# Kernel tuning notes

Hardware: AMD Instinct MI355X
Metric: run time of the kernel (lower is better)

Reference implementation:

```python
import jax, jax.numpy as jnp
import numpy as np

B, C, H, W = 64, 2048, 14, 14
D, S, ITERS, EPS, HID = 256, 8, 3, 1e-8, 512


def build_pos(h, w, d):
    gy, gx = np.meshgrid(np.arange(h), np.arange(w), indexing='ij')
    q = d // 4
    omega = 1.0 / (10000.0 ** (np.arange(q) / q))
    ey = gy.reshape(-1, 1) * omega
    ex = gx.reshape(-1, 1) * omega
    pe = np.concatenate([np.sin(ey), np.cos(ey), np.sin(ex), np.cos(ex)], axis=1)
    return jnp.asarray(pe[None], jnp.float32)  # (1, h*w, d)


def layernorm(x, g, b, eps=1e-5):
    m = x.mean(-1, keepdims=True)
    v = ((x - m) ** 2).mean(-1, keepdims=True)
    return (x - m) * jax.lax.rsqrt(v + eps) * g + b


def setup_inputs() -> dict:
    key = jax.random.key(0)
    ks = jax.random.split(key, 16)
    w = lambda k, shp, s=0.02: jax.random.normal(k, shp, jnp.float32) * s
    inp = {
        'x': jax.random.normal(ks[0], (B, C, H, W), jnp.float32),
        'slot_noise': jax.random.normal(ks[1], (B, S, D), jnp.float32),
        'conv_w': w(ks[2], (C, D)), 'conv_b': jnp.zeros((D,), jnp.float32),
        'pos': build_pos(H, W, D),
        'slots_mu': jax.random.normal(ks[3], (1, 1, D), jnp.float32),
        'slots_logsigma': -jnp.ones((1, 1, D), jnp.float32),
        'qw': w(ks[4], (D, D)), 'qb': jnp.zeros((D,), jnp.float32),
        'kw': w(ks[5], (D, D)), 'kb': jnp.zeros((D,), jnp.float32),
        'vw': w(ks[6], (D, D)), 'vb': jnp.zeros((D,), jnp.float32),
        'gru_wih': w(ks[7], (D, 3 * D)), 'gru_whh': w(ks[8], (D, 3 * D)),
        'gru_bih': jnp.zeros((3 * D,), jnp.float32), 'gru_bhh': jnp.zeros((3 * D,), jnp.float32),
        'w1': w(ks[9], (D, HID)), 'b1': jnp.zeros((HID,), jnp.float32),
        'w2': w(ks[10], (HID, D)), 'b2': jnp.zeros((D,), jnp.float32),
        'ln_in_g': jnp.ones((D,), jnp.float32), 'ln_in_b': jnp.zeros((D,), jnp.float32),
        'ln_s_g': jnp.ones((D,), jnp.float32), 'ln_s_b': jnp.zeros((D,), jnp.float32),
        'ln_ff_g': jnp.ones((D,), jnp.float32), 'ln_ff_b': jnp.zeros((D,), jnp.float32),
    }
    return inp


def reference(x, slot_noise, conv_w, conv_b, pos, slots_mu, slots_logsigma,
              qw, qb, kw, kb, vw, vb, gru_wih, gru_whh, gru_bih, gru_bhh,
              w1, b1, w2, b2, ln_in_g, ln_in_b, ln_s_g, ln_s_b, ln_ff_g, ln_ff_b):
    b, c, h, w_ = x.shape
    d = qw.shape[0]
    scale = d ** (-0.5)
    # (B,C,H,W) -> (B,N,C) -> project -> add pos
    xt = x.transpose(0, 2, 3, 1).reshape(b, h * w_, c)
    xt = xt @ conv_w + conv_b + pos
    # slot init
    slots = slots_mu + jnp.exp(slots_logsigma) * slot_noise  # (B,S,D)
    inp = layernorm(xt, ln_in_g, ln_in_b)
    k = inp @ kw + kb
    v = inp @ vw + vb
    attn = None
    for _ in range(ITERS):
        slots_prev = slots
        s = layernorm(slots, ln_s_g, ln_s_b)
        q = s @ qw + qb
        dots = jnp.einsum('bid,bjd->bij', q, k) * scale  # (B,S,N)
        attn = jax.nn.softmax(dots, axis=1) + EPS  # softmax over slots
        attn = attn / attn.sum(-1, keepdims=True)  # renormalize over keys
        updates = jnp.einsum('bjd,bij->bid', v, attn)  # (B,S,D)
        # GRUCell (torch semantics)
        gi = updates @ gru_wih + gru_bih
        gh = slots_prev @ gru_whh + gru_bhh
        ir, iz, inn = jnp.split(gi, 3, axis=-1)
        hr, hz, hn = jnp.split(gh, 3, axis=-1)
        r = jax.nn.sigmoid(ir + hr)
        z = jax.nn.sigmoid(iz + hz)
        nn_ = jnp.tanh(inn + r * hn)
        slots = (1.0 - z) * nn_ + z * slots_prev
        ff = layernorm(slots, ln_ff_g, ln_ff_b)
        slots = slots + (jax.nn.relu(ff @ w1 + b1)) @ w2 + b2
    attn_map = attn.reshape(b, S, h, w_)
    return slots, attn_map
```

## Files before the change

### kernel.cpp

```cpp
#include <hip/hip_runtime.h>
#include <stdint.h>

#define HWN 196
#define CIN 2048
#define DD  256
#define BB  64
#define NSLOT 8
#define KVPAD 224
#define MTOT 12544
#define BKP 128

typedef __attribute__((ext_vector_type(8))) short short8;
typedef __attribute__((ext_vector_type(4))) float f32x4;
typedef __attribute__((ext_vector_type(4))) unsigned short us4;

__device__ __forceinline__ ushort f2bf(float f){ union{float f;uint32_t u;}v;v.f=f;uint32_t u=v.u;return (ushort)((u+0x7FFFu+((u>>16)&1u))>>16);}
__device__ __forceinline__ float bf2f(ushort h){ union{uint32_t u;float f;}v;v.u=((uint32_t)h)<<16;return v.f;}
__device__ __forceinline__ float sigm(float x){ return 1.f/(1.f+expf(-x)); }

__device__ __forceinline__ short8 ldsY(const ushort* buf, int LD, int kt, int lane){
    int row = lane & 15;
    int ch = kt*4 + (lane>>4);
    return *(const short8*)&buf[row*LD + ((ch ^ (row&7))<<3)];
}
__device__ __forceinline__ short8 gX(const ushort* base, int K, int nrow, int kt, int lane){
    return *(const short8*)&base[(size_t)nrow*K + kt*32 + (lane>>4)*8];
}

struct TD { const float* s; ushort* d; int R, C, t0; };
struct TD8 { TD a[8]; };

__global__ __launch_bounds__(256) void k_prep(TD8 td){
    __shared__ float tile[32][33];
    int bt = blockIdx.x;
    int mi = 0;
    #pragma unroll
    for (int i = 1; i < 8; ++i) if (bt >= td.a[i].t0) mi = i;
    TD d = td.a[mi];
    int lt = bt - d.t0;
    int tilesx = (d.C + 31) >> 5;
    int cb = (lt % tilesx) * 32, rb = (lt / tilesx) * 32;
    int tx = threadIdx.x & 31, ty = threadIdx.x >> 5;
    for (int i = ty; i < 32; i += 8) {
        int r = rb + i, c = cb + tx;
        tile[i][tx] = (r < d.R && c < d.C) ? d.s[(size_t)r * d.C + c] : 0.f;
    }
    __syncthreads();
    for (int i = ty; i < 32; i += 8) {
        int c = cb + i, r = rb + tx;
        if (c < d.C && r < d.R) d.d[(size_t)c * d.R + r] = f2bf(tile[tx][i]);
    }
}

__global__ __launch_bounds__(512) void k_proj(const float* __restrict__ x,
        const ushort* __restrict__ cwT, float* __restrict__ Cpart,
        int SK, int ksteps){
    __shared__ ushort As[2][64*BKP];
    const int t = threadIdx.x, lane = t & 63, wv = t >> 6;
    const int tile = blockIdx.x / SK, kq = blockIdx.x % SK;
    const int bm = tile * 64;
    const int kbase = kq * (ksteps * BKP);

    const int am = t & 63, kg = t >> 6;
    const int mg = bm + am;
    const int ab = mg / HWN, ap = mg % HWN;
    const float* aptr = x + (size_t)ab*(CIN*HWN) + ap + (size_t)kbase*HWN;

    f32x4 acc[4][2] = {};
    float areg[16];

    #pragma unroll
    for (int j = 0; j < 16; ++j) areg[j] = aptr[(size_t)(kg*16+j)*HWN];
    {
        short8 av0, av1;
        #pragma unroll
        for (int j = 0; j < 8; ++j){ av0[j] = (short)f2bf(areg[j]); av1[j] = (short)f2bf(areg[8+j]); }
        int ch0 = kg*2;
        *(short8*)&As[0][am*BKP + ((ch0^(am&7))<<3)] = av0;
        *(short8*)&As[0][am*BKP + (((ch0+1)^(am&7))<<3)] = av1;
    }
    __syncthreads();
    int cur = 0;
    for (int kt = 0; kt < ksteps; ++kt){
        if (kt < ksteps-1){
            #pragma unroll
            for (int j = 0; j < 16; ++j)
                areg[j] = aptr[(size_t)((kt+1)*BKP + kg*16+j)*HWN];
        }
        short8 bfr[4][2];
        #pragma unroll
        for (int kk = 0; kk < 4; ++kk)
            #pragma unroll
            for (int ni = 0; ni < 2; ++ni){
                int n = wv*32 + ni*16 + (lane&15);
                bfr[kk][ni] = *(const short8*)&cwT[(size_t)n*CIN + kbase + kt*BKP + kk*32 + (lane>>4)*8];
            }
        #pragma unroll
        for (int kk = 0; kk < 4; ++kk){
            short8 afr[4];
            #pragma unroll
            for (int mi = 0; mi < 4; ++mi){
                int row = mi*16 + (lane&15);
                int ch = kk*4 + (lane>>4);
                afr[mi] = *(const short8*)&As[cur][row*BKP + ((ch^(row&7))<<3)];
            }
            #pragma unroll
            for (int mi = 0; mi < 4; ++mi)
                #pragma unroll
                for (int ni = 0; ni < 2; ++ni)
                    acc[mi][ni] = __builtin_amdgcn_mfma_f32_16x16x32_bf16(afr[mi], bfr[kk][ni], acc[mi][ni], 0,0,0);
        }
        if (kt < ksteps-1){
            short8 av0, av1;
            #pragma unroll
            for (int j = 0; j < 8; ++j){ av0[j] = (short)f2bf(areg[j]); av1[j] = (short)f2bf(areg[8+j]); }
            int ch0 = kg*2;
            *(short8*)&As[cur^1][am*BKP + ((ch0^(am&7))<<3)] = av0;
            *(short8*)&As[cur^1][am*BKP + (((ch0+1)^(am&7))<<3)] = av1;
        }
        __syncthreads();
        cur ^= 1;
    }
    float* outp = Cpart + (size_t)kq*MTOT*DD;
    #pragma unroll
    for (int mi = 0; mi < 4; ++mi){
        #pragma unroll
        for (int ni = 0; ni < 2; ++ni){
            int n = wv*32 + ni*16 + (lane&15);
            #pragma unroll
            for (int r = 0; r < 4; ++r){
                int m = bm + mi*16 + (lane>>4)*4 + r;
                outp[(size_t)m*DD + n] = acc[mi][ni][r];
            }
        }
    }
}

__global__ __launch_bounds__(512) void k_red(const float* __restrict__ Cpart, int SK,
        const float* __restrict__ cb, const float* __restrict__ pos,
        const float* __restrict__ lng, const float* __restrict__ lnb,
        const ushort* __restrict__ kwT, const ushort* __restrict__ vwT,
        const float* __restrict__ kb, const float* __restrict__ vb,
        ushort* __restrict__ kbf, ushort* __restrict__ vT){
    __shared__ ushort As[32*256];
    const int t = threadIdx.x, lane = t & 63, wv = t >> 6;
    const int b = blockIdx.x / 7, pblk = blockIdx.x % 7;
    {
        int row = t >> 4, seg = t & 15;
        int pin = pblk*32 + row;
        int grow = b*HWN + pin;
        if (grow > MTOT-1) grow = MTOT-1;
        int p = pin < HWN ? pin : HWN-1;
        const float* pp = pos + (size_t)p*DD + seg*16;
        float f[16];
        #pragma unroll
        for (int q = 0; q < 4; ++q){
            f32x4 pv = *(const f32x4*)&pp[q*4];
            f32x4 cv = *(const f32x4*)&cb[seg*16 + q*4];
            #pragma unroll
            for (int r2 = 0; r2 < 4; ++r2) f[q*4+r2] = pv[r2] + cv[r2];
        }
        for (int sk = 0; sk < SK; ++sk){
            const float* cp = Cpart + (size_t)sk*MTOT*DD + (size_t)grow*DD + seg*16;
            #pragma unroll
            for (int q = 0; q < 4; ++q){
                f32x4 a = *(const f32x4*)&cp[q*4];
                #pragma unroll
                for (int r2 = 0; r2 < 4; ++r2) f[q*4+r2] += a[r2];
            }
        }
        float s = 0.f, sq = 0.f;
        #pragma unroll
        for (int j = 0; j < 16; ++j){ s += f[j]; sq += f[j]*f[j]; }
        #pragma unroll
        for (int m = 8; m >= 1; m >>= 1){ s += __shfl_xor(s, m, 64); sq += __shfl_xor(sq, m, 64); }
        float mean = s * (1.f/256.f);
        float rs = rsqrtf(sq*(1.f/256.f) - mean*mean + 1e-5f);
        int d0 = seg*16;
        short8 o0, o1;
        #pragma unroll
        for (int j = 0; j < 8; ++j){
            o0[j] = (short)f2bf((f[j]   - mean)*rs*lng[d0+j]   + lnb[d0+j]);
            o1[j] = (short)f2bf((f[8+j] - mean)*rs*lng[d0+8+j] + lnb[d0+8+j]);
        }
        int ch0 = seg*2;
        *(short8*)&As[row*256 + ((ch0^(row&7))<<3)] = o0;
        *(short8*)&As[row*256 + (((ch0+1)^(row&7))<<3)] = o1;
    }
    __syncthreads();
    f32x4 acck[2][2] = {}, accv[2][2] = {};
    const int n0 = wv*32;
    #pragma unroll
    for (int kt = 0; kt < 8; ++kt){
        short8 afr[2];
        #pragma unroll
        for (int mi = 0; mi < 2; ++mi){
            int row = mi*16 + (lane&15);
            int ch = kt*4 + (lane>>4);
            afr[mi] = *(const short8*)&As[row*256 + ((ch^(row&7))<<3)];
        }
        #pragma unroll
        for (int ni = 0; ni < 2; ++ni){
            int n = n0 + ni*16 + (lane&15);
            int koff = kt*32 + (lane>>4)*8;
            short8 bk = *(const short8*)&kwT[(size_t)n*DD + koff];
            short8 bv = *(const short8*)&vwT[(size_t)n*DD + koff];
            #pragma unroll
            for (int mi = 0; mi < 2; ++mi){
                acck[mi][ni] = __builtin_amdgcn_mfma_f32_16x16x32_bf16(afr[mi], bk, acck[mi][ni],0,0,0);
                accv[mi][ni] = __builtin_amdgcn_mfma_f32_16x16x32_bf16(afr[mi], bv, accv[mi][ni],0,0,0);
            }
        }
    }
    #pragma unroll
    for (int mi = 0; mi < 2; ++mi){
        #pragma unroll
        for (int ni = 0; ni < 2; ++ni){
            int n = n0 + ni*16 + (lane&15);
            float kbn = kb[n], vbn = vb[n];
            int pl0 = pblk*32 + mi*16 + (lane>>4)*4;
            us4 pk;
            #pragma unroll
            for (int r = 0; r < 4; ++r){
                kbf[((size_t)b*KVPAD + pl0 + r)*DD + n] = f2bf(acck[mi][ni][r] + kbn);
                pk[r] = f2bf(accv[mi][ni][r] + vbn);
            }
            *(us4*)&vT[((size_t)b*DD + n)*KVPAD + pl0] = pk;
        }
    }
}

__global__ __launch_bounds__(512) void k_init(const float* __restrict__ noise,
        const float* __restrict__ mu, const float* __restrict__ lsig,
        const ushort* __restrict__ qwT, const float* __restrict__ qb,
        const float* __restrict__ gs, const float* __restrict__ bs,
        float* __restrict__ slots, ushort* __restrict__ qbuf){
    __shared__ float Sld[16*256];
    __shared__ ushort Ysn[16*256];
    __shared__ float part[8][16][2];
    __shared__ float stats[16][2];
    const int t = threadIdx.x, lane = t & 63, w = t >> 6;
    const int bb = blockIdx.x, rbase = bb*16;
    {
        int row = t>>5, ch = t&31; int d = ch*8;
        f32x4 n0 = *(const f32x4*)&noise[(size_t)(rbase+row)*DD + d];
        f32x4 n1 = *(const f32x4*)&noise[(size_t)(rbase+row)*DD + d + 4];
        f32x4 m0 = *(const f32x4*)&mu[d];
        f32x4 m1 = *(const f32x4*)&mu[d+4];
        f32x4 l0 = *(const f32x4*)&lsig[d];
        f32x4 l1 = *(const f32x4*)&lsig[d+4];
        f32x4 s0, s1;
        #pragma unroll
        for (int j = 0; j < 4; ++j){
            s0[j] = m0[j] + expf(l0[j])*n0[j];
            s1[j] = m1[j] + expf(l1[j])*n1[j];
        }
        *(f32x4*)&slots[(size_t)(rbase+row)*DD + d] = s0;
        *(f32x4*)&slots[(size_t)(rbase+row)*DD + d + 4] = s1;
        *(f32x4*)&Sld[row*256 + d] = s0;
        *(f32x4*)&Sld[row*256 + d + 4] = s1;
    }
    __syncthreads();
    f32x4 sv[2];
    #pragma unroll
    for (int sub = 0; sub < 2; ++sub){
        int d0 = w*32 + sub*16 + (lane>>4)*4;
        sv[sub] = *(const f32x4*)&Sld[(lane&15)*256 + d0];
    }
    {
        float lsum = 0.f, lsq = 0.f;
        #pragma unroll
        for (int sub = 0; sub < 2; ++sub)
            #pragma unroll
            for (int r = 0; r < 4; ++r){ float v = sv[sub][r]; lsum += v; lsq += v*v; }
        lsum += __shfl_xor(lsum, 16, 64); lsum += __shfl_xor(lsum, 32, 64);
        lsq  += __shfl_xor(lsq, 16, 64);  lsq  += __shfl_xor(lsq, 32, 64);
        if (lane < 16){ part[w][lane][0] = lsum; part[w][lane][1] = lsq; }
    }
    __syncthreads();
    if (t < 16){
        float a = 0.f, c = 0.f;
        #pragma unroll
        for (int i = 0; i < 8; ++i){ a += part[i][t][0]; c += part[i][t][1]; }
        float mean = a*(1.f/256.f);
        stats[t][0] = mean;
        stats[t][1] = rsqrtf(c*(1.f/256.f) - mean*mean + 1e-5f);
    }
    __syncthreads();
    {
        int slot = lane&15;
        float mean = stats[slot][0], rs = stats[slot][1];
        #pragma unroll
        for (int sub = 0; sub < 2; ++sub){
            int d0 = w*32 + sub*16 + (lane>>4)*4;
            f32x4 g4 = *(const f32x4*)&gs[d0];
            f32x4 b4 = *(const f32x4*)&bs[d0];
            us4 o;
            #pragma unroll
            for (int r = 0; r < 4; ++r) o[r] = f2bf((sv[sub][r]-mean)*rs*g4[r] + b4[r]);
            int ch = d0>>3;
            *(us4*)&Ysn[slot*256 + ((ch^(slot&7))<<3) + (d0&7)] = o;
        }
    }
    __syncthreads();
    f32x4 qa[2] = {};
    #pragma unroll
    for (int kt = 0; kt < 8; ++kt){
        short8 ysn = ldsY(Ysn, 256, kt, lane);
        #pragma unroll
        for (int sub = 0; sub < 2; ++sub){
            int nrow = w*32 + sub*16 + (lane&15);
            short8 xx = gX(qwT, 256, nrow, kt, lane);
            qa[sub] = __builtin_amdgcn_mfma_f32_16x16x32_bf16(xx, ysn, qa[sub], 0,0,0);
        }
    }
    #pragma unroll
    for (int sub = 0; sub < 2; ++sub){
        int qd0 = w*32 + sub*16 + (lane>>4)*4;
        f32x4 qb4 = *(const f32x4*)&qb[qd0];
        us4 o;
        #pragma unroll
        for (int r = 0; r < 4; ++r) o[r] = f2bf((qa[sub][r]+qb4[r])*0.0625f);
        *(us4*)&qbuf[(size_t)(rbase+(lane&15))*DD + qd0] = o;
    }
}

__device__ __forceinline__ float sm_ep(f32x4 acc, int f, int lane, ushort* Xat, int srow){
    int k0 = f*16 + (lane>>4)*4;
    us4 o;
    float ps = 0.f;
    #pragma unroll
    for (int r = 0; r < 4; ++r){
        float v = acc[r];
        float mx = v;
        mx = fmaxf(mx, __shfl_xor(mx, 1, 64));
        mx = fmaxf(mx, __shfl_xor(mx, 2, 64));
        mx = fmaxf(mx, __shfl_xor(mx, 4, 64));
        float e = expf(v - mx);
        float se = e;
        se += __shfl_xor(se, 1, 64);
        se += __shfl_xor(se, 2, 64);
        se += __shfl_xor(se, 4, 64);
        float val = e/se + 1e-8f;
        if (k0 + r >= HWN) val = 0.f;
        ps += val;
        o[r] = f2bf(val);
    }
    int ch = k0 >> 3;
    *(us4*)&Xat[srow*256 + ((ch^(srow&7))<<3) + (k0&7)] = o;
    return ps;
}

__global__ __launch_bounds__(1024, 4) void k_slot(
        const ushort* __restrict__ qbuf, const ushort* __restrict__ kbf,
        const ushort* __restrict__ vT, float* __restrict__ slots,
        ushort* __restrict__ qout,
        const ushort* __restrict__ wihT, const ushort* __restrict__ whhT,
        const float* __restrict__ bih, const float* __restrict__ bhh,
        const ushort* __restrict__ w1T, const float* __restrict__ b1,
        const ushort* __restrict__ w2T, const float* __restrict__ b2,
        const float* __restrict__ gff, const float* __restrict__ bff,
        const float* __restrict__ gs, const float* __restrict__ bs,
        const ushort* __restrict__ qwT, const float* __restrict__ qb,
        float* __restrict__ out_slots, float* __restrict__ out_attn,
        int final_){
    __shared__ ushort Yq[16*256];
    __shared__ ushort Xat[16*256];
    __shared__ ushort Yupd[16*256];
    __shared__ ushort Yslb[16*256];
    __shared__ ushort Ysn[16*256];
    __shared__ ushort Yh[16*512];
    __shared__ float wpart[16][16];
    __shared__ float invk[16];
    __shared__ float part[16][16][2];
    __shared__ float stats[16][2];
    const int t = threadIdx.x, lane = t & 63, w = t >> 6;
    const int b = blockIdx.x;
    const int rbase = b * NSLOT;
    const int srow = lane & 15;
    const int srd = (srow < NSLOT) ? srow : 0;

    if (t < 256){
        int row = t>>5, ch = t&31;
        short8 v = *(const short8*)&qbuf[(size_t)(rbase+row)*DD + ch*8];
        *(short8*)&Yq[row*256 + ((ch^(row&7))<<3)] = v;
        f32x4 s0 = *(const f32x4*)&slots[(size_t)(rbase+row)*DD + ch*8];
        f32x4 s1 = *(const f32x4*)&slots[(size_t)(rbase+row)*DD + ch*8 + 4];
        short8 sv;
        #pragma unroll
        for (int j = 0; j < 4; ++j){ sv[j] = (short)f2bf(s0[j]); sv[4+j] = (short)f2bf(s1[j]); }
        *(short8*)&Yslb[row*256 + ((ch^(row&7))<<3)] = sv;
    } else if (t < 512){
        int i = t - 256;
        int row = (i>>5) + 8, ch = i&31;
        short8 z;
        #pragma unroll
        for (int j = 0; j < 8; ++j) z[j] = 0;
        *(short8*)&Yq[row*256 + ((ch^(row&7))<<3)] = z;
        *(short8*)&Yupd[row*256 + ((ch^(row&7))<<3)] = z;
        *(short8*)&Yslb[row*256 + ((ch^(row&7))<<3)] = z;
    }
    __syncthreads();
    if (w < 14){
        short8 yf[8];
        #pragma unroll
        for (int kt = 0; kt < 8; ++kt) yf[kt] = ldsY(Yq, 256, kt, lane);
        const ushort* kb_ = kbf + (size_t)b*KVPAD*DD;
        const int r0 = w*16 + (lane&15);
        short8 xa[2];
        xa[0] = gX(kb_, 256, r0, 0, lane);
        f32x4 accA = {};
        #pragma unroll
        for (int kt = 0; kt < 8; ++kt){
            int cu = kt & 1, nx = cu ^ 1;
            if (kt < 7) xa[nx] = gX(kb_, 256, r0, kt+1, lane);
            accA = __builtin_amdgcn_mfma_f32_16x16x32_bf16(xa[cu], yf[kt], accA, 0,0,0);
        }
        float ps = sm_ep(accA, w, lane, Xat, srow);
        ps += __shfl_xor(ps, 16, 64);
        ps += __shfl_xor(ps, 32, 64);
        if (lane < 16) wpart[w][lane] = ps;
    } else {
        if (lane < 16) wpart[w][lane] = 0.f;
    }
    __syncthreads();
    if (t < 16){
        float s = 0.f;
        #pragma unroll
        for (int i = 0; i < 16; ++i) s += wpart[i][t];
        invk[t] = 1.f/s;
    }
    f32x4 pv;
    {
        short8 xat[7];
        #pragma unroll
        for (int kt = 0; kt < 7; ++kt) xat[kt] = ldsY(Xat, 256, kt, lane);
        const ushort* vb_ = vT + (size_t)b*DD*KVPAD;
        const int d0r = w*16 + (lane&15);
        short8 ya[2];
        ya[0] = gX(vb_, KVPAD, d0r, 0, lane);
        f32x4 aA = {};
        #pragma unroll
        for (int kt = 0; kt < 7; ++kt){
            int cu = kt & 1, nx = cu ^ 1;
            if (kt < 6) ya[nx] = gX(vb_, KVPAD, d0r, kt+1, lane);
            aA = __builtin_amdgcn_mfma_f32_16x16x32_bf16(xat[kt], ya[cu], aA, 0,0,0);
        }
        pv = aA;
    }
    __syncthreads();
    {
        f32x4 iv = *(const f32x4*)&invk[(lane>>4)*4];
        int d0 = w*16;
        #pragma unroll
        for (int r = 0; r < 4; ++r){
            int s2 = (lane>>4)*4 + r;
            if (s2 < NSLOT){
                int d = d0 + (lane&15);
                int ch = d >> 3;
                Yupd[s2*256 + ((ch^(s2&7))<<3) + (d&7)] = f2bf(pv[r]*iv[r]);
            }
        }
    }
    if (final_){
        for (int idx = t; idx < NSLOT*HWN; idx += 1024){
            int slot = idx/HWN, key = idx - slot*HWN;
            int ch = key >> 3;
            out_attn[(size_t)b*NSLOT*HWN + idx] =
                bf2f(Xat[slot*256 + ((ch^(slot&7))<<3) + (key&7)]) * invk[slot];
        }
    }
    __syncthreads();
    f32x4 gi[3] = {}, gh[3] = {};
    {
        int nrw[3];
        #pragma unroll
        for (int g = 0; g < 3; ++g) nrw[g] = g*256 + w*16 + (lane&15);
        short8 xw[2][6];
        #pragma unroll
        for (int g = 0; g < 3; ++g){
            xw[0][g]   = gX(wihT, 256, nrw[g], 0, lane);
            xw[0][3+g] = gX(whhT, 256, nrw[g], 0, lane);
        }
        #pragma unroll
        for (int kt = 0; kt < 8; ++kt){
            int cu = kt & 1, nx = cu ^ 1;
            if (kt < 7){
                #pragma unroll
                for (int g = 0; g < 3; ++g){
                    xw[nx][g]   = gX(wihT, 256, nrw[g], kt+1, lane);
                    xw[nx][3+g] = gX(whhT, 256, nrw[g], kt+1, lane);
                }
            }
            short8 yu = ldsY(Yupd, 256, kt, lane);
            short8 ys = ldsY(Yslb, 256, kt, lane);
            #pragma unroll
            for (int g = 0; g < 3; ++g){
                gi[g] = __builtin_amdgcn_mfma_f32_16x16x32_bf16(xw[cu][g],   yu, gi[g], 0,0,0);
                gh[g] = __builtin_amdgcn_mfma_f32_16x16x32_bf16(xw[cu][3+g], ys, gh[g], 0,0,0);
            }
        }
    }
    f32x4 snew;
    {
        int d0 = w*16 + (lane>>4)*4;
        f32x4 sp  = *(const f32x4*)&slots[(size_t)(rbase + srd)*DD + d0];
        f32x4 bir = *(const f32x4*)&bih[d0];
        f32x4 biz = *(const f32x4*)&bih[256 + d0];
        f32x4 bin = *(const f32x4*)&bih[512 + d0];
        f32x4 bhr = *(const f32x4*)&bhh[d0];
        f32x4 bhz = *(const f32x4*)&bhh[256 + d0];
        f32x4 bhn = *(const f32x4*)&bhh[512 + d0];
        #pragma unroll
        for (int r = 0; r < 4; ++r){
            float ir = gi[0][r] + bir[r];
            float iz = gi[1][r] + biz[r];
            float in_ = gi[2][r] + bin[r];
            float hr = gh[0][r] + bhr[r];
            float hz = gh[1][r] + bhz[r];
            float hn = gh[2][r] + bhn[r];
            float rr = sigm(ir + hr);
            float zz = sigm(iz + hz);
            float nn = tanhf(in_ + rr*hn);
            snew[r] = (1.f - zz)*nn + zz*sp[r];
        }
    }
    {
        float lsum = 0.f, lsq = 0.f;
        #pragma unroll
        for (int r = 0; r < 4; ++r){ float v = snew[r]; lsum += v; lsq += v*v; }
        lsum += __shfl_xor(lsum, 16, 64); lsum += __shfl_xor(lsum, 32, 64);
        lsq  += __shfl_xor(lsq, 16, 64);  lsq  += __shfl_xor(lsq, 32, 64);
        if (lane < 16){ part[w][lane][0] = lsum; part[w][lane][1] = lsq; }
    }
    __syncthreads();
    if (t < 16){
        float a = 0.f, c = 0.f;
        #pragma unroll
        for (int i = 0; i < 16; ++i){ a += part[i][t][0]; c += part[i][t][1]; }
        float mean = a*(1.f/256.f);
        stats[t][0] = mean;
        stats[t][1] = rsqrtf(c*(1.f/256.f) - mean*mean + 1e-5f);
    }
    __syncthreads();
    {
        float mean = stats[srow][0], rs = stats[srow][1];
        int d0 = w*16 + (lane>>4)*4;
        f32x4 g4 = *(const f32x4*)&gff[d0];
        f32x4 b4 = *(const f32x4*)&bff[d0];
        us4 o;
        #pragma unroll
        for (int r = 0; r < 4; ++r) o[r] = f2bf((snew[r]-mean)*rs*g4[r] + b4[r]);
        int ch = d0 >> 3;
        *(us4*)&Ysn[srow*256 + ((ch^(srow&7))<<3) + (d0&7)] = o;
    }
    __syncthreads();
    {
        int nr1[2];
        #pragma unroll
        for (int s2 = 0; s2 < 2; ++s2) nr1[s2] = w*32 + s2*16 + (lane&15);
        short8 xw1[2][2];
        #pragma unroll
        for (int s2 = 0; s2 < 2; ++s2) xw1[0][s2] = gX(w1T, 256, nr1[s2], 0, lane);
        f32x4 hh[2] = {};
        #pragma unroll
        for (int kt = 0; kt < 8; ++kt){
            int cu = kt & 1, nx = cu ^ 1;
            if (kt < 7){
                #pragma unroll
                for (int s2 = 0; s2 < 2; ++s2) xw1[nx][s2] = gX(w1T, 256, nr1[s2], kt+1, lane);
            }
            short8 ysn = ldsY(Ysn, 256, kt, lane);
            #pragma unroll
            for (int s2 = 0; s2 < 2; ++s2)
                hh[s2] = __builtin_amdgcn_mfma_f32_16x16x32_bf16(xw1[cu][s2], ysn, hh[s2], 0,0,0);
        }
        #pragma unroll
        for (int s2 = 0; s2 < 2; ++s2){
            int n0 = w*32 + s2*16 + (lane>>4)*4;
            f32x4 b14 = *(const f32x4*)&b1[n0];
            us4 o;
            #pragma unroll
            for (int r = 0; r < 4; ++r) o[r] = f2bf(fmaxf(hh[s2][r] + b14[r], 0.f));
            int ch = n0 >> 3;
            *(us4*)&Yh[srow*512 + ((ch^(srow&7))<<3) + (n0&7)] = o;
        }
    }
    __syncthreads();
    f32x4 ns;
    {
        int nr2 = w*16 + (lane&15);
        short8 xw2[2];
        xw2[0] = gX(w2T, 512, nr2, 0, lane);
        f32x4 o2 = {};
        #pragma unroll
        for (int kt = 0; kt < 16; ++kt){
            int cu = kt & 1, nx = cu ^ 1;
            if (kt < 15) xw2[nx] = gX(w2T, 512, nr2, kt+1, lane);
            short8 yh = ldsY(Yh, 512, kt, lane);
            o2 = __builtin_amdgcn_mfma_f32_16x16x32_bf16(xw2[cu], yh, o2, 0,0,0);
        }
        float* dst = final_ ? out_slots : slots;
        int d0 = w*16 + (lane>>4)*4;
        f32x4 b24 = *(const f32x4*)&b2[d0];
        #pragma unroll
        for (int r = 0; r < 4; ++r) ns[r] = o2[r] + b24[r] + snew[r];
        if (srow < NSLOT)
            *(f32x4*)&dst[(size_t)(rbase + srow)*DD + d0] = ns;
    }
    if (final_) return;
    {
        float lsum = 0.f, lsq = 0.f;
        #pragma unroll
        for (int r = 0; r < 4; ++r){ float v = ns[r]; lsum += v; lsq += v*v; }
        lsum += __shfl_xor(lsum, 16, 64); lsum += __shfl_xor(lsum, 32, 64);
        lsq  += __shfl_xor(lsq, 16, 64);  lsq  += __shfl_xor(lsq, 32, 64);
        if (lane < 16){ part[w][lane][0] = lsum; part[w][lane][1] = lsq; }
    }
    __syncthreads();
    if (t < 16){
        float a = 0.f, c = 0.f;
        #pragma unroll
        for (int i = 0; i < 16; ++i){ a += part[i][t][0]; c += part[i][t][1]; }
        float mean = a*(1.f/256.f);
        stats[t][0] = mean;
        stats[t][1] = rsqrtf(c*(1.f/256.f) - mean*mean + 1e-5f);
    }
    __syncthreads();
    {
        float mean = stats[srow][0], rs = stats[srow][1];
        int d0 = w*16 + (lane>>4)*4;
        f32x4 g4 = *(const f32x4*)&gs[d0];
        f32x4 b4 = *(const f32x4*)&bs[d0];
        us4 o;
        #pragma unroll
        for (int r = 0; r < 4; ++r) o[r] = f2bf((ns[r]-mean)*rs*g4[r] + b4[r]);
        int ch = d0 >> 3;
        *(us4*)&Ysn[srow*256 + ((ch^(srow&7))<<3) + (d0&7)] = o;
    }
    __syncthreads();
    {
        int nrq = w*16 + (lane&15);
        short8 xq[2];
        xq[0] = gX(qwT, 256, nrq, 0, lane);
        f32x4 qa = {};
        #pragma unroll
        for (int kt = 0; kt < 8; ++kt){
            int cu = kt & 1, nx = cu ^ 1;
            if (kt < 7) xq[nx] = gX(qwT, 256, nrq, kt+1, lane);
            short8 ysn = ldsY(Ysn, 256, kt, lane);
            qa = __builtin_amdgcn_mfma_f32_16x16x32_bf16(xq[cu], ysn, qa, 0,0,0);
        }
        int qd0 = w*16 + (lane>>4)*4;
        f32x4 qb4 = *(const f32x4*)&qb[qd0];
        us4 o;
        #pragma unroll
        for (int r = 0; r < 4; ++r) o[r] = f2bf((qa[r]+qb4[r])*0.0625f);
        if (srow < NSLOT)
            *(us4*)&qout[(size_t)(rbase + srow)*DD + qd0] = o;
    }
}

extern "C" void kernel_launch(void* const* d_in, const int* in_sizes, int n_in,
                              void* d_out, int out_size, void* d_ws, size_t ws_size,
                              hipStream_t stream) {
    const float* x      = (const float*)d_in[0];
    const float* noise  = (const float*)d_in[1];
    const float* conv_w = (const float*)d_in[2];
    const float* conv_b = (const float*)d_in[3];
    const float* pos    = (const float*)d_in[4];
    const float* mu     = (const float*)d_in[5];
    const float* logsig = (const float*)d_in[6];
    const float* qw  = (const float*)d_in[7];
    const float* qb  = (const float*)d_in[8];
    const float* kw  = (const float*)d_in[9];
    const float* kb  = (const float*)d_in[10];
    const float* vw  = (const float*)d_in[11];
    const float* vb  = (const float*)d_in[12];
    const float* wih = (const float*)d_in[13];
    const float* whh = (const float*)d_in[14];
    const float* bih = (const float*)d_in[15];
    const float* bhh = (const float*)d_in[16];
    const float* w1  = (const float*)d_in[17];
    const float* b1  = (const float*)d_in[18];
    const float* w2  = (const float*)d_in[19];
    const float* b2  = (const float*)d_in[20];
    const float* g_in = (const float*)d_in[21];
    const float* b_in = (const float*)d_in[22];
    const float* g_s  = (const float*)d_in[23];
    const float* b_s  = (const float*)d_in[24];
    const float* g_ff = (const float*)d_in[25];
    const float* b_ff = (const float*)d_in[26];

    char* w = (char*)d_ws;
    ushort* kbf    = (ushort*)w; w += (size_t)BB*KVPAD*DD*2;
    ushort* vT     = (ushort*)w; w += (size_t)BB*DD*KVPAD*2;
    ushort* cwT    = (ushort*)w; w += (size_t)DD*CIN*2;
    ushort* qwT    = (ushort*)w; w += (size_t)DD*DD*2;
    ushort* kwT    = (ushort*)w; w += (size_t)DD*DD*2;
    ushort* vwT    = (ushort*)w; w += (size_t)DD*DD*2;
    ushort* wihT   = (ushort*)w; w += (size_t)768*DD*2;
    ushort* whhT   = (ushort*)w; w += (size_t)768*DD*2;
    ushort* w1T    = (ushort*)w; w += (size_t)512*DD*2;
    ushort* w2T    = (ushort*)w; w += (size_t)DD*512*2;
    ushort* qbb    = (ushort*)w; w += (size_t)BB*NSLOT*DD*2;
    float*  slotsb = (float*)w;  w += (size_t)BB*NSLOT*DD*4;
    float*  Cpart  = (float*)w;
    size_t fixedBytes = (size_t)(w - (char*)d_ws);
    int SK = (fixedBytes + (size_t)4*MTOT*DD*4 <= ws_size) ? 4 : 2;
    int ksteps = 16 / SK;

    float* out_slots = (float*)d_out;
    float* out_attn  = (float*)d_out + (size_t)BB*NSLOT*DD;

    TD8 td;
    td.a[0] = { conv_w, cwT, 2048, 256,    0 };
    td.a[1] = { qw,     qwT,  256, 256,  512 };
    td.a[2] = { kw,     kwT,  256, 256,  576 };
    td.a[3] = { vw,     vwT,  256, 256,  640 };
    td.a[4] = { wih,    wihT, 256, 768,  704 };
    td.a[5] = { whh,    whhT, 256, 768,  896 };
    td.a[6] = { w1,     w1T,  256, 512, 1088 };
    td.a[7] = { w2,     w2T,  512, 256, 1216 };

    k_prep<<<1344, 256, 0, stream>>>(td);
    k_proj<<<196*SK, 512, 0, stream>>>(x, cwT, Cpart, SK, ksteps);
    k_red<<<448, 512, 0, stream>>>(Cpart, SK, conv_b, pos, g_in, b_in,
                                   kwT, vwT, kb, vb, kbf, vT);
    k_init<<<32, 512, 0, stream>>>(noise, mu, logsig, qwT, qb, g_s, b_s, slotsb, qbb);
    for (int it = 0; it < 3; ++it){
        k_slot<<<BB, 1024, 0, stream>>>(qbb, kbf, vT, slotsb, qbb,
                                        wihT, whhT, bih, bhh, w1T, b1, w2T, b2,
                                        g_ff, b_ff, g_s, b_s, qwT, qb,
                                        out_slots, out_attn, it == 2);
    }
}
```

Before: 243.5 us.

## Replace split-K projection with N-tiled GEMM and merge kv/init kernels

The conv projection GEMM no longer splits K and writes fp32 partials. It tiles over N in two 128-wide halves, runs the full K loop, and writes a bf16 xt with bias and positional encoding already added. The K/V layernorm-projection kernel and the slot-init kernel are merged into one launch. In k_slot, several stats and inverse-sum stages now compute redundantly per thread, which removes __syncthreads, and the occupancy hint is lowered. This cuts partial-sum traffic and a launch, but drops the register double-buffering in k_proj and adds bf16 rounding of xt before the layernorm.

```diff
diff --git a/kernel.cpp b/kernel.cpp
--- a/kernel.cpp
+++ b/kernel.cpp
@@ -8,7 +8,6 @@
 #define NSLOT 8
 #define KVPAD 224
 #define MTOT 12544
-#define BKP 128
 
 typedef __attribute__((ext_vector_type(8))) short short8;
 typedef __attribute__((ext_vector_type(4))) float f32x4;
@@ -52,276 +51,260 @@
     }
 }
 
-__global__ __launch_bounds__(512) void k_proj(const float* __restrict__ x,
-        const ushort* __restrict__ cwT, float* __restrict__ Cpart,
-        int SK, int ksteps){
-    __shared__ ushort As[2][64*BKP];
-    const int t = threadIdx.x, lane = t & 63, wv = t >> 6;
-    const int tile = blockIdx.x / SK, kq = blockIdx.x % SK;
-    const int bm = tile * 64;
-    const int kbase = kq * (ksteps * BKP);
-
-    const int am = t & 63, kg = t >> 6;
+__global__ __launch_bounds__(256) void k_proj(const float* __restrict__ x,
+        const ushort* __restrict__ bT, const float* __restrict__ cb,
+        const float* __restrict__ pos, ushort* __restrict__ xt){
+    __shared__ ushort As[64 * 64];
+    __shared__ ushort Bs[128 * 64];
+    const int t = threadIdx.x;
+    const int lane = t & 63;
+    const int wv = t >> 6;
+    const int wm = wv >> 1, wn = wv & 1;
+    const int bm = blockIdx.x * 64;
+    const int bn = blockIdx.y * 128;
+
+    const int am = t & 63;
     const int mg = bm + am;
     const int ab = mg / HWN, ap = mg % HWN;
-    const float* aptr = x + (size_t)ab*(CIN*HWN) + ap + (size_t)kbase*HWN;
-
-    f32x4 acc[4][2] = {};
-    float areg[16];
-
+    const float* aptr = x + (size_t)ab * (CIN * HWN) + ap;
+    const int achb = t >> 6;
+
+    const int bnl = t >> 1;
+    const int bch0 = (t & 1) * 4;
+    const ushort* bptr = bT + (size_t)(bn + bnl) * CIN;
+
+    f32x4 acc[2][4] = {};
+
+    for (int k0 = 0; k0 < CIN; k0 += 64) {
+        if (k0) __syncthreads();
+        #pragma unroll
+        for (int p = 0; p < 2; ++p) {
+            int ch = achb + 4 * p;
+            short8 av;
+            #pragma unroll
+            for (int j = 0; j < 8; ++j)
+                av[j] = (short)f2bf(aptr[(size_t)(k0 + ch * 8 + j) * HWN]);
+            *(short8*)&As[am * 64 + ((ch ^ (am & 7)) << 3)] = av;
+        }
+        #pragma unroll
+        for (int c = 0; c < 4; ++c) {
+            int ch = bch0 + c;
+            short8 bv = *(const short8*)&bptr[k0 + ch * 8];
+            *(short8*)&Bs[bnl * 64 + ((ch ^ (bnl & 7)) << 3)] = bv;
+        }
+        __syncthreads();
+        #pragma unroll
+        for (int kk = 0; kk < 2; ++kk) {
+            short8 afr[2], bfr[4];
+            #pragma unroll
+            for (int mi = 0; mi < 2; ++mi) {
+                int row = wm * 32 + mi * 16 + (lane & 15);
+                int ch = kk * 4 + (lane >> 4);
+                afr[mi] = *(const short8*)&As[row * 64 + ((ch ^ (row & 7)) << 3)];
+            }
+            #pragma unroll
+            for (int ni = 0; ni < 4; ++ni) {
+                int row = wn * 64 + ni * 16 + (lane & 15);
+                int ch = kk * 4 + (lane >> 4);
+                bfr[ni] = *(const short8*)&Bs[row * 64 + ((ch ^ (row & 7)) << 3)];
+            }
+            #pragma unroll
+            for (int mi = 0; mi < 2; ++mi)
+                #pragma unroll
+                for (int ni = 0; ni < 4; ++ni)
+                    acc[mi][ni] = __builtin_amdgcn_mfma_f32_16x16x32_bf16(
+                        afr[mi], bfr[ni], acc[mi][ni], 0, 0, 0);
+        }
+    }
     #pragma unroll
-    for (int j = 0; j < 16; ++j) areg[j] = aptr[(size_t)(kg*16+j)*HWN];
-    {
-        short8 av0, av1;
-        #pragma unroll
-        for (int j = 0; j < 8; ++j){ av0[j] = (short)f2bf(areg[j]); av1[j] = (short)f2bf(areg[8+j]); }
-        int ch0 = kg*2;
-        *(short8*)&As[0][am*BKP + ((ch0^(am&7))<<3)] = av0;
-        *(short8*)&As[0][am*BKP + (((ch0+1)^(am&7))<<3)] = av1;
-    }
-    __syncthreads();
-    int cur = 0;
-    for (int kt = 0; kt < ksteps; ++kt){
-        if (kt < ksteps-1){
-            #pragma unroll
-            for (int j = 0; j < 16; ++j)
-                areg[j] = aptr[(size_t)((kt+1)*BKP + kg*16+j)*HWN];
-        }
-        short8 bfr[4][2];
-        #pragma unroll
-        for (int kk = 0; kk < 4; ++kk)
-            #pragma unroll
-            for (int ni = 0; ni < 2; ++ni){
-                int n = wv*32 + ni*16 + (lane&15);
-                bfr[kk][ni] = *(const short8*)&cwT[(size_t)n*CIN + kbase + kt*BKP + kk*32 + (lane>>4)*8];
-            }
-        #pragma unroll
-        for (int kk = 0; kk < 4; ++kk){
-            short8 afr[4];
-            #pragma unroll
-            for (int mi = 0; mi < 4; ++mi){
-                int row = mi*16 + (lane&15);
-                int ch = kk*4 + (lane>>4);
-                afr[mi] = *(const short8*)&As[cur][row*BKP + ((ch^(row&7))<<3)];
-            }
-            #pragma unroll
-            for (int mi = 0; mi < 4; ++mi)
-                #pragma unroll
-                for (int ni = 0; ni < 2; ++ni)
-                    acc[mi][ni] = __builtin_amdgcn_mfma_f32_16x16x32_bf16(afr[mi], bfr[kk][ni], acc[mi][ni], 0,0,0);
-        }
-        if (kt < ksteps-1){
-            short8 av0, av1;
-            #pragma unroll
-            for (int j = 0; j < 8; ++j){ av0[j] = (short)f2bf(areg[j]); av1[j] = (short)f2bf(areg[8+j]); }
-            int ch0 = kg*2;
-            *(short8*)&As[cur^1][am*BKP + ((ch0^(am&7))<<3)] = av0;
-            *(short8*)&As[cur^1][am*BKP + (((ch0+1)^(am&7))<<3)] = av1;
-        }
-        __syncthreads();
-        cur ^= 1;
-    }
-    float* outp = Cpart + (size_t)kq*MTOT*DD;
-    #pragma unroll
-    for (int mi = 0; mi < 4; ++mi){
-        #pragma unroll
-        for (int ni = 0; ni < 2; ++ni){
-            int n = wv*32 + ni*16 + (lane&15);
-            #pragma unroll
-            for (int r = 0; r < 4; ++r){
-                int m = bm + mi*16 + (lane>>4)*4 + r;
-                outp[(size_t)m*DD + n] = acc[mi][ni][r];
+    for (int mi = 0; mi < 2; ++mi) {
+        #pragma unroll
+        for (int ni = 0; ni < 4; ++ni) {
+            int n = bn + wn * 64 + ni * 16 + (lane & 15);
+            float cbn = cb[n];
+            #pragma unroll
+            for (int r = 0; r < 4; ++r) {
+                int row = wm * 32 + mi * 16 + (lane >> 4) * 4 + r;
+                int m = bm + row;
+                int p = m % HWN;
+                xt[(size_t)m * DD + n] = f2bf(acc[mi][ni][r] + cbn + pos[(size_t)p * DD + n]);
             }
         }
     }
 }
 
-__global__ __launch_bounds__(512) void k_red(const float* __restrict__ Cpart, int SK,
-        const float* __restrict__ cb, const float* __restrict__ pos,
-        const float* __restrict__ lng, const float* __restrict__ lnb,
+__global__ __launch_bounds__(512) void k_kvinit(const ushort* __restrict__ xt,
         const ushort* __restrict__ kwT, const ushort* __restrict__ vwT,
         const float* __restrict__ kb, const float* __restrict__ vb,
-        ushort* __restrict__ kbf, ushort* __restrict__ vT){
-    __shared__ ushort As[32*256];
-    const int t = threadIdx.x, lane = t & 63, wv = t >> 6;
-    const int b = blockIdx.x / 7, pblk = blockIdx.x % 7;
-    {
-        int row = t >> 4, seg = t & 15;
-        int pin = pblk*32 + row;
-        int grow = b*HWN + pin;
-        if (grow > MTOT-1) grow = MTOT-1;
-        int p = pin < HWN ? pin : HWN-1;
-        const float* pp = pos + (size_t)p*DD + seg*16;
-        float f[16];
-        #pragma unroll
-        for (int q = 0; q < 4; ++q){
-            f32x4 pv = *(const f32x4*)&pp[q*4];
-            f32x4 cv = *(const f32x4*)&cb[seg*16 + q*4];
-            #pragma unroll
-            for (int r2 = 0; r2 < 4; ++r2) f[q*4+r2] = pv[r2] + cv[r2];
-        }
-        for (int sk = 0; sk < SK; ++sk){
-            const float* cp = Cpart + (size_t)sk*MTOT*DD + (size_t)grow*DD + seg*16;
-            #pragma unroll
-            for (int q = 0; q < 4; ++q){
-                f32x4 a = *(const f32x4*)&cp[q*4];
-                #pragma unroll
-                for (int r2 = 0; r2 < 4; ++r2) f[q*4+r2] += a[r2];
-            }
-        }
-        float s = 0.f, sq = 0.f;
-        #pragma unroll
-        for (int j = 0; j < 16; ++j){ s += f[j]; sq += f[j]*f[j]; }
-        #pragma unroll
-        for (int m = 8; m >= 1; m >>= 1){ s += __shfl_xor(s, m, 64); sq += __shfl_xor(sq, m, 64); }
-        float mean = s * (1.f/256.f);
-        float rs = rsqrtf(sq*(1.f/256.f) - mean*mean + 1e-5f);
-        int d0 = seg*16;
-        short8 o0, o1;
-        #pragma unroll
-        for (int j = 0; j < 8; ++j){
-            o0[j] = (short)f2bf((f[j]   - mean)*rs*lng[d0+j]   + lnb[d0+j]);
-            o1[j] = (short)f2bf((f[8+j] - mean)*rs*lng[d0+8+j] + lnb[d0+8+j]);
-        }
-        int ch0 = seg*2;
-        *(short8*)&As[row*256 + ((ch0^(row&7))<<3)] = o0;
-        *(short8*)&As[row*256 + (((ch0+1)^(row&7))<<3)] = o1;
-    }
-    __syncthreads();
-    f32x4 acck[2][2] = {}, accv[2][2] = {};
-    const int n0 = wv*32;
-    #pragma unroll
-    for (int kt = 0; kt < 8; ++kt){
-        short8 afr[2];
-        #pragma unroll
-        for (int mi = 0; mi < 2; ++mi){
-            int row = mi*16 + (lane&15);
-            int ch = kt*4 + (lane>>4);
-            afr[mi] = *(const short8*)&As[row*256 + ((ch^(row&7))<<3)];
-        }
-        #pragma unroll
-        for (int ni = 0; ni < 2; ++ni){
-            int n = n0 + ni*16 + (lane&15);
-            int koff = kt*32 + (lane>>4)*8;
-            short8 bk = *(const short8*)&kwT[(size_t)n*DD + koff];
-            short8 bv = *(const short8*)&vwT[(size_t)n*DD + koff];
-            #pragma unroll
-            for (int mi = 0; mi < 2; ++mi){
-                acck[mi][ni] = __builtin_amdgcn_mfma_f32_16x16x32_bf16(afr[mi], bk, acck[mi][ni],0,0,0);
-                accv[mi][ni] = __builtin_amdgcn_mfma_f32_16x16x32_bf16(afr[mi], bv, accv[mi][ni],0,0,0);
-            }
-        }
-    }
-    #pragma unroll
-    for (int mi = 0; mi < 2; ++mi){
-        #pragma unroll
-        for (int ni = 0; ni < 2; ++ni){
-            int n = n0 + ni*16 + (lane&15);
-            float kbn = kb[n], vbn = vb[n];
-            int pl0 = pblk*32 + mi*16 + (lane>>4)*4;
-            us4 pk;
-            #pragma unroll
-            for (int r = 0; r < 4; ++r){
-                kbf[((size_t)b*KVPAD + pl0 + r)*DD + n] = f2bf(acck[mi][ni][r] + kbn);
-                pk[r] = f2bf(accv[mi][ni][r] + vbn);
-            }
-            *(us4*)&vT[((size_t)b*DD + n)*KVPAD + pl0] = pk;
-        }
-    }
-}
-
-__global__ __launch_bounds__(512) void k_init(const float* __restrict__ noise,
-        const float* __restrict__ mu, const float* __restrict__ lsig,
+        const float* __restrict__ lng, const float* __restrict__ lnb,
+        ushort* __restrict__ kbf, ushort* __restrict__ vT,
+        const float* __restrict__ noise, const float* __restrict__ mu,
+        const float* __restrict__ lsig,
         const ushort* __restrict__ qwT, const float* __restrict__ qb,
         const float* __restrict__ gs, const float* __restrict__ bs,
         float* __restrict__ slots, ushort* __restrict__ qbuf){
+    __shared__ ushort As[32*256];
     __shared__ float Sld[16*256];
-    __shared__ ushort Ysn[16*256];
     __shared__ float part[8][16][2];
     __shared__ float stats[16][2];
-    const int t = threadIdx.x, lane = t & 63, w = t >> 6;
-    const int bb = blockIdx.x, rbase = bb*16;
-    {
-        int row = t>>5, ch = t&31; int d = ch*8;
-        f32x4 n0 = *(const f32x4*)&noise[(size_t)(rbase+row)*DD + d];
-        f32x4 n1 = *(const f32x4*)&noise[(size_t)(rbase+row)*DD + d + 4];
-        f32x4 m0 = *(const f32x4*)&mu[d];
-        f32x4 m1 = *(const f32x4*)&mu[d+4];
-        f32x4 l0 = *(const f32x4*)&lsig[d];
-        f32x4 l1 = *(const f32x4*)&lsig[d+4];
-        f32x4 s0, s1;
-        #pragma unroll
-        for (int j = 0; j < 4; ++j){
-            s0[j] = m0[j] + expf(l0[j])*n0[j];
-            s1[j] = m1[j] + expf(l1[j])*n1[j];
-        }
-        *(f32x4*)&slots[(size_t)(rbase+row)*DD + d] = s0;
-        *(f32x4*)&slots[(size_t)(rbase+row)*DD + d + 4] = s1;
-        *(f32x4*)&Sld[row*256 + d] = s0;
-        *(f32x4*)&Sld[row*256 + d + 4] = s1;
-    }
-    __syncthreads();
-    f32x4 sv[2];
-    #pragma unroll
-    for (int sub = 0; sub < 2; ++sub){
-        int d0 = w*32 + sub*16 + (lane>>4)*4;
-        sv[sub] = *(const f32x4*)&Sld[(lane&15)*256 + d0];
-    }
-    {
-        float lsum = 0.f, lsq = 0.f;
-        #pragma unroll
-        for (int sub = 0; sub < 2; ++sub)
-            #pragma unroll
-            for (int r = 0; r < 4; ++r){ float v = sv[sub][r]; lsum += v; lsq += v*v; }
-        lsum += __shfl_xor(lsum, 16, 64); lsum += __shfl_xor(lsum, 32, 64);
-        lsq  += __shfl_xor(lsq, 16, 64);  lsq  += __shfl_xor(lsq, 32, 64);
-        if (lane < 16){ part[w][lane][0] = lsum; part[w][lane][1] = lsq; }
-    }
-    __syncthreads();
-    if (t < 16){
-        float a = 0.f, c = 0.f;
-        #pragma unroll
-        for (int i = 0; i < 8; ++i){ a += part[i][t][0]; c += part[i][t][1]; }
-        float mean = a*(1.f/256.f);
-        stats[t][0] = mean;
-        stats[t][1] = rsqrtf(c*(1.f/256.f) - mean*mean + 1e-5f);
-    }
-    __syncthreads();
-    {
-        int slot = lane&15;
-        float mean = stats[slot][0], rs = stats[slot][1];
+    const int t = threadIdx.x, lane = t & 63, wv = t >> 6;
+    if (blockIdx.x < 448){
+        const int b = blockIdx.x / 7, pblk = blockIdx.x % 7;
+        {
+            int row = t >> 4, seg = t & 15;
+            int grow = b*HWN + pblk*32 + row;
+            if (grow > MTOT-1) grow = MTOT-1;
+            const ushort* src = &xt[(size_t)grow*DD + seg*16];
+            short8 v0 = *(const short8*)&src[0];
+            short8 v1 = *(const short8*)&src[8];
+            float f[16];
+            #pragma unroll
+            for (int j = 0; j < 8; ++j){ f[j] = bf2f((ushort)v0[j]); f[8+j] = bf2f((ushort)v1[j]); }
+            float s = 0.f, sq = 0.f;
+            #pragma unroll
+            for (int j = 0; j < 16; ++j){ s += f[j]; sq += f[j]*f[j]; }
+            #pragma unroll
+            for (int m = 8; m >= 1; m >>= 1){ s += __shfl_xor(s, m, 64); sq += __shfl_xor(sq, m, 64); }
+            float mean = s * (1.f/256.f);
+            float rs = rsqrtf(sq*(1.f/256.f) - mean*mean + 1e-5f);
+            int d0 = seg*16;
+            short8 o0, o1;
+            #pragma unroll
+            for (int j = 0; j < 8; ++j){
+                o0[j] = (short)f2bf((f[j]   - mean)*rs*lng[d0+j]   + lnb[d0+j]);
+                o1[j] = (short)f2bf((f[8+j] - mean)*rs*lng[d0+8+j] + lnb[d0+8+j]);
+            }
+            int ch0 = seg*2;
+            *(short8*)&As[row*256 + ((ch0^(row&7))<<3)] = o0;
+            *(short8*)&As[row*256 + (((ch0+1)^(row&7))<<3)] = o1;
+        }
+        __syncthreads();
+        f32x4 acck[2][2] = {}, accv[2][2] = {};
+        const int n0 = wv*32;
+        #pragma unroll
+        for (int kt = 0; kt < 8; ++kt){
+            short8 afr[2];
+            #pragma unroll
+            for (int mi = 0; mi < 2; ++mi){
+                int row = mi*16 + (lane&15);
+                int ch = kt*4 + (lane>>4);
+                afr[mi] = *(const short8*)&As[row*256 + ((ch^(row&7))<<3)];
+            }
+            #pragma unroll
+            for (int ni = 0; ni < 2; ++ni){
+                int n = n0 + ni*16 + (lane&15);
+                int koff = kt*32 + (lane>>4)*8;
+                short8 bk = *(const short8*)&kwT[(size_t)n*DD + koff];
+                short8 bv = *(const short8*)&vwT[(size_t)n*DD + koff];
+                #pragma unroll
+                for (int mi = 0; mi < 2; ++mi){
+                    acck[mi][ni] = __builtin_amdgcn_mfma_f32_16x16x32_bf16(afr[mi], bk, acck[mi][ni],0,0,0);
+                    accv[mi][ni] = __builtin_amdgcn_mfma_f32_16x16x32_bf16(afr[mi], bv, accv[mi][ni],0,0,0);
+                }
+            }
+        }
+        #pragma unroll
+        for (int mi = 0; mi < 2; ++mi){
+            #pragma unroll
+            for (int ni = 0; ni < 2; ++ni){
+                int n = n0 + ni*16 + (lane&15);
+                float kbn = kb[n], vbn = vb[n];
+                int pl0 = pblk*32 + mi*16 + (lane>>4)*4;
+                us4 pk;
+                #pragma unroll
+                for (int r = 0; r < 4; ++r){
+                    kbf[((size_t)b*KVPAD + pl0 + r)*DD + n] = f2bf(acck[mi][ni][r] + kbn);
+                    pk[r] = f2bf(accv[mi][ni][r] + vbn);
+                }
+                *(us4*)&vT[((size_t)b*DD + n)*KVPAD + pl0] = pk;
+            }
+        }
+    } else {
+        ushort* Ysn = As;
+        const int bb = blockIdx.x - 448, rbase = bb*16;
+        const int w = wv;
+        {
+            int row = t>>5, ch = t&31; int d = ch*8;
+            f32x4 n0 = *(const f32x4*)&noise[(size_t)(rbase+row)*DD + d];
+            f32x4 n1 = *(const f32x4*)&noise[(size_t)(rbase+row)*DD + d + 4];
+            f32x4 m0 = *(const f32x4*)&mu[d];
+            f32x4 m1 = *(const f32x4*)&mu[d+4];
+            f32x4 l0 = *(const f32x4*)&lsig[d];
+            f32x4 l1 = *(const f32x4*)&lsig[d+4];
+            f32x4 s0, s1;
+            #pragma unroll
+            for (int j = 0; j < 4; ++j){
+                s0[j] = m0[j] + expf(l0[j])*n0[j];
+                s1[j] = m1[j] + expf(l1[j])*n1[j];
+            }
+            *(f32x4*)&slots[(size_t)(rbase+row)*DD + d] = s0;
+            *(f32x4*)&slots[(size_t)(rbase+row)*DD + d + 4] = s1;
+            *(f32x4*)&Sld[row*256 + d] = s0;
+            *(f32x4*)&Sld[row*256 + d + 4] = s1;
+        }
+        __syncthreads();
+        f32x4 sv[2];
         #pragma unroll
         for (int sub = 0; sub < 2; ++sub){
             int d0 = w*32 + sub*16 + (lane>>4)*4;
-            f32x4 g4 = *(const f32x4*)&gs[d0];
-            f32x4 b4 = *(const f32x4*)&bs[d0];
+            sv[sub] = *(const f32x4*)&Sld[(lane&15)*256 + d0];
+        }
+        {
+            float lsum = 0.f, lsq = 0.f;
+            #pragma unroll
+            for (int sub = 0; sub < 2; ++sub)
+                #pragma unroll
+                for (int r = 0; r < 4; ++r){ float v = sv[sub][r]; lsum += v; lsq += v*v; }
+            lsum += __shfl_xor(lsum, 16, 64); lsum += __shfl_xor(lsum, 32, 64);
+            lsq  += __shfl_xor(lsq, 16, 64);  lsq  += __shfl_xor(lsq, 32, 64);
+            if (lane < 16){ part[w][lane][0] = lsum; part[w][lane][1] = lsq; }
+        }
+        __syncthreads();
+        if (t < 16){
+            float a = 0.f, c = 0.f;
+            #pragma unroll
+            for (int i = 0; i < 8; ++i){ a += part[i][t][0]; c += part[i][t][1]; }
+            float mean = a*(1.f/256.f);
+            stats[t][0] = mean;
+            stats[t][1] = rsqrtf(c*(1.f/256.f) - mean*mean + 1e-5f);
+        }
+        __syncthreads();
+        {
+            int slot = lane&15;
+            float mean = stats[slot][0], rs = stats[slot][1];
+            #pragma unroll
+            for (int sub = 0; sub < 2; ++sub){
+                int d0 = w*32 + sub*16 + (lane>>4)*4;
+                f32x4 g4 = *(const f32x4*)&gs[d0];
+                f32x4 b4 = *(const f32x4*)&bs[d0];
+                us4 o;
+                #pragma unroll
+                for (int r = 0; r < 4; ++r) o[r] = f2bf((sv[sub][r]-mean)*rs*g4[r] + b4[r]);
+                int ch = d0>>3;
+                *(us4*)&Ysn[slot*256 + ((ch^(slot&7))<<3) + (d0&7)] = o;
+            }
+        }
+        __syncthreads();
+        f32x4 qa[2] = {};
+        #pragma unroll
+        for (int kt = 0; kt < 8; ++kt){
+            short8 ysn = ldsY(Ysn, 256, kt, lane);
+            #pragma unroll
+            for (int sub = 0; sub < 2; ++sub){
+                int nrow = w*32 + sub*16 + (lane&15);
+                short8 xx = gX(qwT, 256, nrow, kt, lane);
+                qa[sub] = __builtin_amdgcn_mfma_f32_16x16x32_bf16(xx, ysn, qa[sub], 0,0,0);
+            }
+        }
+        #pragma unroll
+        for (int sub = 0; sub < 2; ++sub){
+            int qd0 = w*32 + sub*16 + (lane>>4)*4;
+            f32x4 qb4 = *(const f32x4*)&qb[qd0];
             us4 o;
             #pragma unroll
-            for (int r = 0; r < 4; ++r) o[r] = f2bf((sv[sub][r]-mean)*rs*g4[r] + b4[r]);
-            int ch = d0>>3;
-            *(us4*)&Ysn[slot*256 + ((ch^(slot&7))<<3) + (d0&7)] = o;
-        }
-    }
-    __syncthreads();
-    f32x4 qa[2] = {};
-    #pragma unroll
-    for (int kt = 0; kt < 8; ++kt){
-        short8 ysn = ldsY(Ysn, 256, kt, lane);
-        #pragma unroll
-        for (int sub = 0; sub < 2; ++sub){
-            int nrow = w*32 + sub*16 + (lane&15);
-            short8 xx = gX(qwT, 256, nrow, kt, lane);
-            qa[sub] = __builtin_amdgcn_mfma_f32_16x16x32_bf16(xx, ysn, qa[sub], 0,0,0);
-        }
-    }
-    #pragma unroll
-    for (int sub = 0; sub < 2; ++sub){
-        int qd0 = w*32 + sub*16 + (lane>>4)*4;
-        f32x4 qb4 = *(const f32x4*)&qb[qd0];
-        us4 o;
-        #pragma unroll
-        for (int r = 0; r < 4; ++r) o[r] = f2bf((qa[sub][r]+qb4[r])*0.0625f);
-        *(us4*)&qbuf[(size_t)(rbase+(lane&15))*DD + qd0] = o;
+            for (int r = 0; r < 4; ++r) o[r] = f2bf((qa[sub][r]+qb4[r])*0.0625f);
+            *(us4*)&qbuf[(size_t)(rbase+(lane&15))*DD + qd0] = o;
+        }
     }
 }
 
@@ -351,7 +334,7 @@
     return ps;
 }
 
-__global__ __launch_bounds__(1024, 4) void k_slot(
+__global__ __launch_bounds__(1024, 2) void k_slot(
         const ushort* __restrict__ qbuf, const ushort* __restrict__ kbf,
         const ushort* __restrict__ vT, float* __restrict__ slots,
         ushort* __restrict__ qout,
@@ -371,9 +354,7 @@
     __shared__ ushort Ysn[16*256];
     __shared__ ushort Yh[16*512];
     __shared__ float wpart[16][16];
-    __shared__ float invk[16];
     __shared__ float part[16][16][2];
-    __shared__ float stats[16][2];
     const int t = threadIdx.x, lane = t & 63, w = t >> 6;
     const int b = blockIdx.x;
     const int rbase = b * NSLOT;
@@ -424,12 +405,6 @@
         if (lane < 16) wpart[w][lane] = 0.f;
     }
     __syncthreads();
-    if (t < 16){
-        float s = 0.f;
-        #pragma unroll
-        for (int i = 0; i < 16; ++i) s += wpart[i][t];
-        invk[t] = 1.f/s;
-    }
     f32x4 pv;
     {
         short8 xat[7];
@@ -448,9 +423,16 @@
         }
         pv = aA;
     }
-    __syncthreads();
-    {
-        f32x4 iv = *(const f32x4*)&invk[(lane>>4)*4];
+    {
+        f32x4 iv;
+        #pragma unroll
+        for (int r = 0; r < 4; ++r){
+            int s2 = (lane>>4)*4 + r;
+            float s = 0.f;
+            #pragma unroll
+            for (int i = 0; i < 16; ++i) s += wpart[i][s2];
+            iv[r] = 1.f/s;
+        }
         int d0 = w*16;
         #pragma unroll
         for (int r = 0; r < 4; ++r){
@@ -465,9 +447,12 @@
     if (final_){
         for (int idx = t; idx < NSLOT*HWN; idx += 1024){
             int slot = idx/HWN, key = idx - slot*HWN;
+            float s = 0.f;
+            #pragma unroll
+            for (int i = 0; i < 16; ++i) s += wpart[i][slot];
             int ch = key >> 3;
             out_attn[(size_t)b*NSLOT*HWN + idx] =
-                bf2f(Xat[slot*256 + ((ch^(slot&7))<<3) + (key&7)]) * invk[slot];
+                bf2f(Xat[slot*256 + ((ch^(slot&7))<<3) + (key&7)]) / s;
         }
     }
     __syncthreads();
@@ -534,17 +519,12 @@
         if (lane < 16){ part[w][lane][0] = lsum; part[w][lane][1] = lsq; }
     }
     __syncthreads();
-    if (t < 16){
+    {
         float a = 0.f, c = 0.f;
         #pragma unroll
-        for (int i = 0; i < 16; ++i){ a += part[i][t][0]; c += part[i][t][1]; }
+        for (int i = 0; i < 16; ++i){ a += part[i][srow][0]; c += part[i][srow][1]; }
         float mean = a*(1.f/256.f);
-        stats[t][0] = mean;
-        stats[t][1] = rsqrtf(c*(1.f/256.f) - mean*mean + 1e-5f);
-    }
-    __syncthreads();
-    {
-        float mean = stats[srow][0], rs = stats[srow][1];
+        float rs = rsqrtf(c*(1.f/256.f) - mean*mean + 1e-5f);
         int d0 = w*16 + (lane>>4)*4;
         f32x4 g4 = *(const f32x4*)&gff[d0];
         f32x4 b4 = *(const f32x4*)&bff[d0];
@@ -618,17 +598,12 @@
         if (lane < 16){ part[w][lane][0] = lsum; part[w][lane][1] = lsq; }
     }
     __syncthreads();
-    if (t < 16){
+    {
         float a = 0.f, c = 0.f;
         #pragma unroll
-        for (int i = 0; i < 16; ++i){ a += part[i][t][0]; c += part[i][t][1]; }
+        for (int i = 0; i < 16; ++i){ a += part[i][srow][0]; c += part[i][srow][1]; }
         float mean = a*(1.f/256.f);
-        stats[t][0] = mean;
-        stats[t][1] = rsqrtf(c*(1.f/256.f) - mean*mean + 1e-5f);
-    }
-    __syncthreads();
-    {
-        float mean = stats[srow][0], rs = stats[srow][1];
+        float rs = rsqrtf(c*(1.f/256.f) - mean*mean + 1e-5f);
         int d0 = w*16 + (lane>>4)*4;
         f32x4 g4 = *(const f32x4*)&gs[d0];
         f32x4 b4 = *(const f32x4*)&bs[d0];
@@ -705,10 +680,7 @@
     ushort* w2T    = (ushort*)w; w += (size_t)DD*512*2;
     ushort* qbb    = (ushort*)w; w += (size_t)BB*NSLOT*DD*2;
     float*  slotsb = (float*)w;  w += (size_t)BB*NSLOT*DD*4;
-    float*  Cpart  = (float*)w;
-    size_t fixedBytes = (size_t)(w - (char*)d_ws);
-    int SK = (fixedBytes + (size_t)4*MTOT*DD*4 <= ws_size) ? 4 : 2;
-    int ksteps = 16 / SK;
+    ushort* xt     = (ushort*)w; w += (size_t)MTOT*DD*2;
 
     float* out_slots = (float*)d_out;
     float* out_attn  = (float*)d_out + (size_t)BB*NSLOT*DD;
@@ -724,10 +696,10 @@
     td.a[7] = { w2,     w2T,  512, 256, 1216 };
 
     k_prep<<<1344, 256, 0, stream>>>(td);
-    k_proj<<<196*SK, 512, 0, stream>>>(x, cwT, Cpart, SK, ksteps);
-    k_red<<<448, 512, 0, stream>>>(Cpart, SK, conv_b, pos, g_in, b_in,
-                                   kwT, vwT, kb, vb, kbf, vT);
-    k_init<<<32, 512, 0, stream>>>(noise, mu, logsig, qwT, qb, g_s, b_s, slotsb, qbb);
+    k_proj<<<dim3(196, 2), 256, 0, stream>>>(x, cwT, conv_b, pos, xt);
+    k_kvinit<<<480, 512, 0, stream>>>(xt, kwT, vwT, kb, vb, g_in, b_in, kbf, vT,
+                                      noise, mu, logsig, qwT, qb, g_s, b_s,
+                                      slotsb, qbb);
     for (int it = 0; it < 3; ++it){
         k_slot<<<BB, 1024, 0, stream>>>(qbb, kbf, vT, slotsb, qbb,
                                         wihT, whhT, bih, bhh, w1T, b1, w2T, b2,
```

Result: faster. 225.6 us (-7.4%).
